# Kernel tuning notes

Hardware: AMD Instinct MI355X
Metric: run time of the kernel (lower is better)

## Reference

```python
import jax, jax.numpy as jnp
import numpy as np

N_NODES = 50000
N_EDGES = 1600000
N_GRAPHS = 1000


def setup_inputs() -> dict:
    key = jax.random.key(0)
    ks = jax.random.split(key, 16)
    s = 0.1
    return {
        "x": jax.random.normal(ks[0], (N_NODES, 7), jnp.float32),
        "edge_attr": jax.random.normal(ks[1], (N_EDGES, 4), jnp.float32),
        "edge_index": jax.random.randint(ks[2], (2, N_EDGES), 0, N_NODES),
        "batch": jnp.sort(jax.random.randint(ks[3], (N_NODES,), 0, N_GRAPHS)),
        "We1": jax.random.normal(ks[4], (4, 7), jnp.float32) * s,
        "be1": jnp.zeros((7,), jnp.float32),
        "W1a": jax.random.normal(ks[5], (7, 64), jnp.float32) * s,
        "b1a": jnp.zeros((64,), jnp.float32),
        "W1b": jax.random.normal(ks[6], (64, 64), jnp.float32) * s,
        "b1b": jnp.zeros((64,), jnp.float32),
        "We2": jax.random.normal(ks[7], (4, 64), jnp.float32) * s,
        "be2": jnp.zeros((64,), jnp.float32),
        "W2a": jax.random.normal(ks[8], (64, 64), jnp.float32) * s,
        "b2a": jnp.zeros((64,), jnp.float32),
        "W2b": jax.random.normal(ks[9], (64, 64), jnp.float32) * s,
        "b2b": jnp.zeros((64,), jnp.float32),
        "Wfc": jax.random.normal(ks[10], (64, 12), jnp.float32) * s,
        "bfc": jnp.zeros((12,), jnp.float32),
    }


def _gine_conv(h, edge_attr, src, dst, We, be, Wa, ba, Wb, bb, n_nodes):
    # GINEConv (eps=0): out = nn(h + sum_j relu(h[src] + lin(edge_attr)))
    e = edge_attr @ We + be                      # [E, d]
    msg = jax.nn.relu(h[src] + e)                # [E, d] gather + add + relu
    aggr = jax.ops.segment_sum(msg, dst, num_segments=n_nodes)  # scatter-sum
    z = h + aggr
    return jax.nn.relu(z @ Wa + ba) @ Wb + bb


def reference(x, edge_attr, edge_index, batch,
              We1, be1, W1a, b1a, W1b, b1b,
              We2, be2, W2a, b2a, W2b, b2b,
              Wfc, bfc):
    src, dst = edge_index[0], edge_index[1]
    n = x.shape[0]
    h = jax.nn.relu(_gine_conv(x, edge_attr, src, dst, We1, be1, W1a, b1a, W1b, b1b, n))
    h = jax.nn.relu(_gine_conv(h, edge_attr, src, dst, We2, be2, W2a, b2a, W2b, b2b, n))
    # global mean pool over batch index
    sums = jax.ops.segment_sum(h, batch, num_segments=N_GRAPHS)          # [G, 64]
    cnt = jax.ops.segment_sum(jnp.ones((n,), h.dtype), batch, num_segments=N_GRAPHS)
    pooled = sums / jnp.maximum(cnt, 1.0)[:, None]
    return pooled @ Wfc + bfc                                            # [G, 12]
```

## Files before the change

kernel.cpp:

```cpp
#include <hip/hip_runtime.h>

typedef unsigned char uchar;
typedef unsigned short ushort;
typedef unsigned int uint;

constexpr int NN = 50000;
constexpr int NE = 1600000;
constexpr int NG = 1000;
constexpr int NB2 = 196;
constexpr int TILE = 4096;
constexpr int NTILE = (NE + TILE - 1) / TILE;
constexpr int SPAN_CAP = 9216;
constexpr int MSTRIDE = 72;
constexpr int NPB = 16;
constexpr int NBLK2 = NN / NPB;

constexpr int OFF_BCNT  = 0;
constexpr int OFF_SUMS  = 256;
constexpr int OFF_CNT   = 64256;
constexpr int ZERO_UNITS= 65280;
constexpr int OFF_BBASE = 65280;
constexpr int OFF_BCUR  = 65536;
constexpr int OFF_OFFS  = 65792;
constexpr int OFF_P0    = 116224;
constexpr int OFF_P1    = 1716224;
constexpr int OFF_P2    = 3316224;
constexpr int OFF_Z1    = 4916224;
constexpr int OFF_H1    = 5316224;
constexpr int OFF_Z     = 6916224;

typedef __attribute__((ext_vector_type(8))) short short8;
typedef __attribute__((ext_vector_type(4))) float float4v;
typedef __attribute__((ext_vector_type(2))) float float2v;

__device__ __forceinline__ uint f2bf(float f) {
    uint u = __float_as_uint(f);
    return (u + 0x7fffu + ((u >> 16) & 1u)) >> 16;
}
__device__ __forceinline__ float bf2f_lo(uint p) { return __uint_as_float(p << 16); }
__device__ __forceinline__ float bf2f_hi(uint p) { return __uint_as_float(p & 0xffff0000u); }

__global__ __launch_bounds__(256) void bhist_kernel(const int* __restrict__ eidx,
                                                    int* __restrict__ bcnt) {
    __shared__ int lh[NB2];
    for (int i = threadIdx.x; i < NB2; i += 256) lh[i] = 0;
    __syncthreads();
    int tid = blockIdx.x * 256 + threadIdx.x;
    int stride = gridDim.x * 256;
    for (int e = tid; e < NE; e += stride) atomicAdd(&lh[eidx[NE + e] >> 8], 1);
    __syncthreads();
    for (int i = threadIdx.x; i < NB2; i += 256) if (lh[i]) atomicAdd(&bcnt[i], lh[i]);
}

__global__ __launch_bounds__(256) void bscan_kernel(const int* __restrict__ bcnt,
                                                    int* __restrict__ bbase,
                                                    int* __restrict__ bcur) {
    __shared__ int s[256];
    int t = threadIdx.x;
    int v = (t < NB2) ? bcnt[t] : 0;
    s[t] = v; __syncthreads();
    for (int o = 1; o < 256; o <<= 1) {
        int u = (t >= o) ? s[t - o] : 0;
        __syncthreads();
        s[t] += u;
        __syncthreads();
    }
    bbase[t] = s[t] - v;
    bcur[t] = s[t] - v;
}

__global__ __launch_bounds__(256) void bin_kernel(const int* __restrict__ eidx,
                                                  const float4* __restrict__ ea,
                                                  int* __restrict__ bcur,
                                                  uint* __restrict__ p0,
                                                  uint* __restrict__ p1,
                                                  uint* __restrict__ p2) {
    __shared__ uint s0[TILE], s1[TILE], s2[TILE];
    __shared__ int hcnt[NB2], hoff[NB2 + 1], hcur[NB2], gbase[NB2];
    const int t = threadIdx.x;
    const int e0 = blockIdx.x * TILE;
    const int cnt = (NE - e0 < TILE) ? (NE - e0) : TILE;
    for (int i = t; i < NB2; i += 256) hcnt[i] = 0;
    __syncthreads();
    int dsts[16];
    #pragma unroll
    for (int k = 0; k < 16; ++k) {
        int i = t + k * 256;
        int d = (i < cnt) ? eidx[NE + e0 + i] : -1;
        dsts[k] = d;
        if (d >= 0) atomicAdd(&hcnt[d >> 8], 1);
    }
    __syncthreads();
    if (t == 0) {
        int a = 0;
        for (int b = 0; b < NB2; ++b) { hoff[b] = a; a += hcnt[b]; }
        hoff[NB2] = a;
    }
    __syncthreads();
    if (t < NB2) { hcur[t] = hoff[t]; gbase[t] = atomicAdd(&bcur[t], hcnt[t]); }
    __syncthreads();
    #pragma unroll
    for (int k = 0; k < 16; ++k) {
        int d = dsts[k];
        if (d < 0) continue;
        int i = t + k * 256;
        int e = e0 + i;
        int src = eidx[e];
        float4 a = ea[e];
        int bkt = d >> 8;
        int lp = atomicAdd(&hcur[bkt], 1);
        s0[lp] = (uint)src | ((uint)(d & 255) << 16) | ((uint)bkt << 24);
        s1[lp] = f2bf(a.x) | (f2bf(a.y) << 16);
        s2[lp] = f2bf(a.z) | (f2bf(a.w) << 16);
    }
    __syncthreads();
    for (int i = t; i < cnt; i += 256) {
        uint r0 = s0[i];
        int bkt = (int)(r0 >> 24);
        int gp = gbase[bkt] + (i - hoff[bkt]);
        p0[gp] = r0; p1[gp] = s1[i]; p2[gp] = s2[i];
    }
}

__global__ __launch_bounds__(256) void build_kernel(const int* __restrict__ bbase,
                                                    const int* __restrict__ bcnt,
                                                    int* __restrict__ offs,
                                                    uint* __restrict__ p0,
                                                    uint* __restrict__ p1,
                                                    uint* __restrict__ p2) {
    __shared__ uint s0[SPAN_CAP], s1[SPAN_CAP], s2[SPAN_CAP];
    __shared__ int ldeg[256], lcur[256], sscan[256];
    const int t = threadIdx.x;
    const int b = blockIdx.x;
    const int nlo = b << 8;
    const int base = bbase[b];
    int span = bcnt[b];
    if (span > SPAN_CAP) span = SPAN_CAP;
    ldeg[t] = 0;
    __syncthreads();
    for (int i = t; i < span; i += 256)
        atomicAdd(&ldeg[(p0[base + i] >> 16) & 0xFFu], 1);
    __syncthreads();
    int v = ldeg[t];
    sscan[t] = v; __syncthreads();
    for (int o = 1; o < 256; o <<= 1) {
        int u = (t >= o) ? sscan[t - o] : 0;
        __syncthreads();
        sscan[t] += u;
        __syncthreads();
    }
    int exc = sscan[t] - v;
    lcur[t] = exc;
    int gi = nlo + t;
    if (gi < NN) offs[gi] = base + exc;
    else if (gi < 50176) offs[gi] = NE;
    __syncthreads();
    for (int i = t; i < span; i += 256) {
        uint r0 = p0[base + i], r1 = p1[base + i], r2 = p2[base + i];
        int pos = atomicAdd(&lcur[(r0 >> 16) & 0xFFu], 1);
        s0[pos] = r0; s1[pos] = r1; s2[pos] = r2;
    }
    __syncthreads();
    for (int i = t; i < span; i += 256) {
        p0[base + i] = s0[i]; p1[base + i] = s1[i]; p2[base + i] = s2[i];
    }
}

__global__ __launch_bounds__(256) void xpack_kernel(const float* __restrict__ x,
                                                    float* __restrict__ xp) {
    int i = blockIdx.x * 256 + threadIdx.x;
    if (i < NN * 8) {
        int n = i >> 3, c = i & 7;
        xp[i] = (c < 7) ? x[n * 7 + c] : 0.f;
    }
}

__global__ __launch_bounds__(256) void aggr1_kernel(
    const float* __restrict__ xp,
    const uint* __restrict__ p0, const uint* __restrict__ p1, const uint* __restrict__ p2,
    const int* __restrict__ offs,
    const float* __restrict__ We1, const float* __restrict__ be1,
    float* __restrict__ z1)
{
    const int tid = threadIdx.x;
    const int lane = tid & 63;
    const int wv = tid >> 6;
    const int grp = lane >> 2;
    const int cl = lane & 3;
    const int n = blockIdx.x * 64 + wv * 16 + grp;

    float2v wE[4], bE;
    const bool c1ok = (2 * cl + 1 < 7);
    #pragma unroll
    for (int k = 0; k < 4; ++k) {
        wE[k][0] = We1[k * 7 + 2 * cl];
        wE[k][1] = c1ok ? We1[k * 7 + 2 * cl + 1] : 0.f;
    }
    bE[0] = be1[2 * cl];
    bE[1] = c1ok ? be1[2 * cl + 1] : 0.f;

    const int off = offs[n];
    const int deg = offs[n + 1] - off;
    const int degm1 = (deg > 0) ? deg - 1 : 0;
    const int offC = (deg > 0) ? off : 0;
    int dmax = deg;
    dmax = max(dmax, __shfl_xor(dmax, 4));
    dmax = max(dmax, __shfl_xor(dmax, 8));
    dmax = max(dmax, __shfl_xor(dmax, 16));
    dmax = max(dmax, __shfl_xor(dmax, 32));

    float2v acc = {0.f, 0.f};
    const float2v zero2 = {0.f, 0.f};
    int j = 0;
    for (; j + 2 <= dmax; j += 2) {
        const bool q0 = (j < deg), q1 = (j + 1 < deg);
        const int e0 = offC + (q0 ? j : degm1);
        const int e1 = offC + (q1 ? j + 1 : degm1);
        const uint r00 = p0[e0], ry0 = p1[e0], rz0 = p2[e0];
        const uint r01 = p0[e1], ry1 = p1[e1], rz1 = p2[e1];
        const float2v xg0 = *(const float2v*)&xp[((size_t)(r00 & 0xFFFFu) << 3) + 2 * cl];
        const float2v xg1 = *(const float2v*)&xp[((size_t)(r01 & 0xFFFFu) << 3) + 2 * cl];
        {
            float2v ev = bE + bf2f_lo(ry0) * wE[0] + bf2f_hi(ry0) * wE[1]
                       + bf2f_lo(rz0) * wE[2] + bf2f_hi(rz0) * wE[3];
            float2v tv = xg0 + ev;
            tv[0] = fmaxf(tv[0], 0.f);
            tv[1] = fmaxf(tv[1], 0.f);
            acc += q0 ? tv : zero2;
        }
        {
            float2v ev = bE + bf2f_lo(ry1) * wE[0] + bf2f_hi(ry1) * wE[1]
                       + bf2f_lo(rz1) * wE[2] + bf2f_hi(rz1) * wE[3];
            float2v tv = xg1 + ev;
            tv[0] = fmaxf(tv[0], 0.f);
            tv[1] = fmaxf(tv[1], 0.f);
            acc += q1 ? tv : zero2;
        }
    }
    if (j < dmax) {
        const bool q0 = (j < deg);
        const int e0 = offC + (q0 ? j : degm1);
        const uint r00 = p0[e0], ry0 = p1[e0], rz0 = p2[e0];
        const float2v xg0 = *(const float2v*)&xp[((size_t)(r00 & 0xFFFFu) << 3) + 2 * cl];
        float2v ev = bE + bf2f_lo(ry0) * wE[0] + bf2f_hi(ry0) * wE[1]
                   + bf2f_lo(rz0) * wE[2] + bf2f_hi(rz0) * wE[3];
        float2v tv = xg0 + ev;
        tv[0] = fmaxf(tv[0], 0.f);
        tv[1] = fmaxf(tv[1], 0.f);
        acc += q0 ? tv : zero2;
    }

    if (n < NN) {
        const float2v xn = *(const float2v*)&xp[(size_t)n * 8 + 2 * cl];
        float2v zv = xn + acc;
        *(float2v*)&z1[(size_t)n * 8 + 2 * cl] = zv;
    }
}

__global__ __launch_bounds__(256) void node1_kernel(
    const float* __restrict__ z1,
    const float* __restrict__ W1a, const float* __restrict__ b1a,
    const float* __restrict__ W1b, const float* __restrict__ b1b,
    uint* __restrict__ h1u)
{
    __shared__ __align__(16) ushort sT[64 * MSTRIDE];
    __shared__ __align__(16) ushort sO[64 * 64];
    const int t = threadIdx.x;
    const int w = t >> 6, lane = t & 63;
    const int qm = lane & 15, quad = lane >> 4;
    const int n0 = blockIdx.x * 64;
    const int node = n0 + w * 16 + qm;

    short8 wa1n[4];
    #pragma unroll
    for (int nt = 0; nt < 4; ++nt) {
        short8 v = (short8)0;
        if (quad == 0) {
            #pragma unroll
            for (int j = 0; j < 7; ++j)
                v[j] = (short)f2bf(W1a[j * 64 + nt * 16 + qm]);
        }
        wa1n[nt] = v;
    }
    short8 wb1[2][4];
    #pragma unroll
    for (int s = 0; s < 2; ++s)
        #pragma unroll
        for (int nt = 0; nt < 4; ++nt) {
            short8 v;
            #pragma unroll
            for (int j = 0; j < 8; ++j)
                v[j] = (short)f2bf(W1b[(s * 32 + quad * 8 + j) * 64 + nt * 16 + qm]);
            wb1[s][nt] = v;
        }
    float ba[4], bb[4];
    #pragma unroll
    for (int nt = 0; nt < 4; ++nt) { ba[nt] = b1a[nt * 16 + qm]; bb[nt] = b1b[nt * 16 + qm]; }

    short8 af1 = (short8)0;
    if (quad == 0 && node < NN) {
        const float4 za = *(const float4*)(z1 + (size_t)node * 8);
        const float4 zbv = *(const float4*)(z1 + (size_t)node * 8 + 4);
        af1[0] = (short)f2bf(za.x); af1[1] = (short)f2bf(za.y);
        af1[2] = (short)f2bf(za.z); af1[3] = (short)f2bf(za.w);
        af1[4] = (short)f2bf(zbv.x); af1[5] = (short)f2bf(zbv.y);
        af1[6] = (short)f2bf(zbv.z); af1[7] = (short)f2bf(zbv.w);
    }
    float4v acc[4];
    #pragma unroll
    for (int nt = 0; nt < 4; ++nt) {
        acc[nt] = (float4v){0.f, 0.f, 0.f, 0.f};
        acc[nt] = __builtin_amdgcn_mfma_f32_16x16x32_bf16(af1, wa1n[nt], acc[nt], 0, 0, 0);
    }
    #pragma unroll
    for (int nt = 0; nt < 4; ++nt)
        #pragma unroll
        for (int r = 0; r < 4; ++r)
            sT[(w * 16 + quad * 4 + r) * MSTRIDE + nt * 16 + qm] =
                (ushort)f2bf(fmaxf(acc[nt][r] + ba[nt], 0.f));
    __syncthreads();

    #pragma unroll
    for (int nt = 0; nt < 4; ++nt) acc[nt] = (float4v){0.f, 0.f, 0.f, 0.f};
    #pragma unroll
    for (int s = 0; s < 2; ++s) {
        short8 af = *(const short8*)&sT[(w * 16 + qm) * MSTRIDE + s * 32 + quad * 8];
        #pragma unroll
        for (int nt = 0; nt < 4; ++nt)
            acc[nt] = __builtin_amdgcn_mfma_f32_16x16x32_bf16(af, wb1[s][nt], acc[nt], 0, 0, 0);
    }
    #pragma unroll
    for (int nt = 0; nt < 4; ++nt)
        #pragma unroll
        for (int r = 0; r < 4; ++r)
            sO[(w * 16 + quad * 4 + r) * 64 + nt * 16 + qm] =
                (ushort)f2bf(fmaxf(acc[nt][r] + bb[nt], 0.f));
    __syncthreads();
    for (int i = t; i < 64 * 32; i += 256) {
        int nd = i >> 5;
        if (n0 + nd < NN) h1u[(size_t)(n0 + nd) * 32 + (i & 31)] = ((const uint*)sO)[i];
    }
}

__global__ __launch_bounds__(256) void aggr2_kernel(
    const uint* __restrict__ h1u,
    const uint* __restrict__ p0, const uint* __restrict__ p1, const uint* __restrict__ p2,
    const int* __restrict__ offs,
    const float* __restrict__ We2, const float* __restrict__ be2,
    uint* __restrict__ zb)
{
    const int tid = threadIdx.x;
    const int lane = tid & 63;
    const int wv = tid >> 6;
    const int grp = lane >> 4;
    const int cl = lane & 15;
    const int n = blockIdx.x * NPB + wv * 4 + grp;

    float2v wA[4], wB[4], bA, bB;
    #pragma unroll
    for (int k = 0; k < 4; ++k) {
        const float4 w4 = *(const float4*)&We2[k * 64 + 4 * cl];
        wA[k][0] = w4.x; wA[k][1] = w4.y;
        wB[k][0] = w4.z; wB[k][1] = w4.w;
    }
    {
        const float4 b4 = *(const float4*)&be2[4 * cl];
        bA[0] = b4.x; bA[1] = b4.y;
        bB[0] = b4.z; bB[1] = b4.w;
    }

    const int off = offs[n];
    const int deg = offs[n + 1] - off;
    const int degm1 = (deg > 0) ? deg - 1 : 0;
    const int offC = (deg > 0) ? off : 0;
    int dmax = deg;
    dmax = max(dmax, __shfl_xor(dmax, 16));
    dmax = max(dmax, __shfl_xor(dmax, 32));

    float2v accA = {0.f, 0.f}, accB = {0.f, 0.f};
    const float2v zero2 = {0.f, 0.f};
    int j = 0;
    for (; j + 2 <= dmax; j += 2) {
        const bool q0 = (j < deg), q1 = (j + 1 < deg);
        const int e0 = offC + (q0 ? j : degm1);
        const int e1 = offC + (q1 ? j + 1 : degm1);
        const uint r00 = p0[e0], ry0 = p1[e0], rz0 = p2[e0];
        const uint r01 = p0[e1], ry1 = p1[e1], rz1 = p2[e1];
        const uint2 g0 = *(const uint2*)&h1u[((size_t)(r00 & 0xFFFFu) << 5) + 2 * cl];
        const uint2 g1 = *(const uint2*)&h1u[((size_t)(r01 & 0xFFFFu) << 5) + 2 * cl];
        {
            float2v bvA = bA + bf2f_lo(ry0) * wA[0] + bf2f_hi(ry0) * wA[1]
                        + bf2f_lo(rz0) * wA[2] + bf2f_hi(rz0) * wA[3];
            float2v bvB = bB + bf2f_lo(ry0) * wB[0] + bf2f_hi(ry0) * wB[1]
                        + bf2f_lo(rz0) * wB[2] + bf2f_hi(rz0) * wB[3];
            float2v tA, tB;
            tA[0] = fmaxf(bf2f_lo(g0.x) + bvA[0], 0.f);
            tA[1] = fmaxf(bf2f_hi(g0.x) + bvA[1], 0.f);
            tB[0] = fmaxf(bf2f_lo(g0.y) + bvB[0], 0.f);
            tB[1] = fmaxf(bf2f_hi(g0.y) + bvB[1], 0.f);
            accA += q0 ? tA : zero2;
            accB += q0 ? tB : zero2;
        }
        {
            float2v bvA = bA + bf2f_lo(ry1) * wA[0] + bf2f_hi(ry1) * wA[1]
                        + bf2f_lo(rz1) * wA[2] + bf2f_hi(rz1) * wA[3];
            float2v bvB = bB + bf2f_lo(ry1) * wB[0] + bf2f_hi(ry1) * wB[1]
                        + bf2f_lo(rz1) * wB[2] + bf2f_hi(rz1) * wB[3];
            float2v tA, tB;
            tA[0] = fmaxf(bf2f_lo(g1.x) + bvA[0], 0.f);
            tA[1] = fmaxf(bf2f_hi(g1.x) + bvA[1], 0.f);
            tB[0] = fmaxf(bf2f_lo(g1.y) + bvB[0], 0.f);
            tB[1] = fmaxf(bf2f_hi(g1.y) + bvB[1], 0.f);
            accA += q1 ? tA : zero2;
            accB += q1 ? tB : zero2;
        }
    }
    if (j < dmax) {
        const bool q0 = (j < deg);
        const int e0 = offC + (q0 ? j : degm1);
        const uint r00 = p0[e0], ry0 = p1[e0], rz0 = p2[e0];
        const uint2 g0 = *(const uint2*)&h1u[((size_t)(r00 & 0xFFFFu) << 5) + 2 * cl];
        float2v bvA = bA + bf2f_lo(ry0) * wA[0] + bf2f_hi(ry0) * wA[1]
                    + bf2f_lo(rz0) * wA[2] + bf2f_hi(rz0) * wA[3];
        float2v bvB = bB + bf2f_lo(ry0) * wB[0] + bf2f_hi(ry0) * wB[1]
                    + bf2f_lo(rz0) * wB[2] + bf2f_hi(rz0) * wB[3];
        float2v tA, tB;
        tA[0] = fmaxf(bf2f_lo(g0.x) + bvA[0], 0.f);
        tA[1] = fmaxf(bf2f_hi(g0.x) + bvA[1], 0.f);
        tB[0] = fmaxf(bf2f_lo(g0.y) + bvB[0], 0.f);
        tB[1] = fmaxf(bf2f_hi(g0.y) + bvB[1], 0.f);
        accA += q0 ? tA : zero2;
        accB += q0 ? tB : zero2;
    }

    const uint2 hw = *(const uint2*)&h1u[(size_t)n * 32 + 2 * cl];
    uint o0 = f2bf(bf2f_lo(hw.x) + accA[0]) | (f2bf(bf2f_hi(hw.x) + accA[1]) << 16);
    uint o1 = f2bf(bf2f_lo(hw.y) + accB[0]) | (f2bf(bf2f_hi(hw.y) + accB[1]) << 16);
    uint2 ov; ov.x = o0; ov.y = o1;
    *(uint2*)&zb[(size_t)n * 32 + 2 * cl] = ov;
}

__global__ __launch_bounds__(256) void mlp2_kernel(
    const uint* __restrict__ zb,
    const float* __restrict__ W2a, const float* __restrict__ b2a,
    const float* __restrict__ W2b, const float* __restrict__ b2b,
    const int* __restrict__ batch,
    float* __restrict__ sums, float* __restrict__ cnt)
{
    __shared__ __align__(16) ushort sT[64 * MSTRIDE];
    __shared__ float sH[64 * 64];
    __shared__ int sB[64];
    __shared__ float pbuf[4][64];
    __shared__ int pcnt[4];
    const int t = threadIdx.x;
    const int w = t >> 6, lane = t & 63;
    const int qm = lane & 15, quad = lane >> 4;
    const int n0 = blockIdx.x * 64;
    const int node = n0 + w * 16 + qm;
    const int nv = (NN - n0 < 64) ? (NN - n0) : 64;

    if (t < 64) sB[t] = (n0 + t < NN) ? batch[n0 + t] : -2;

    short8 wa[2][4], wb[2][4];
    #pragma unroll
    for (int s = 0; s < 2; ++s)
        #pragma unroll
        for (int nt = 0; nt < 4; ++nt) {
            short8 va, vb;
            #pragma unroll
            for (int j = 0; j < 8; ++j) {
                int k = s * 32 + quad * 8 + j, n = nt * 16 + qm;
                va[j] = (short)f2bf(W2a[k * 64 + n]);
                vb[j] = (short)f2bf(W2b[k * 64 + n]);
            }
            wa[s][nt] = va; wb[s][nt] = vb;
        }
    float ba[4], bb[4];
    #pragma unroll
    for (int nt = 0; nt < 4; ++nt) { ba[nt] = b2a[nt * 16 + qm]; bb[nt] = b2b[nt * 16 + qm]; }

    float4v acc[4];
    #pragma unroll
    for (int nt = 0; nt < 4; ++nt) acc[nt] = (float4v){0.f, 0.f, 0.f, 0.f};
    #pragma unroll
    for (int s = 0; s < 2; ++s) {
        uint4 zw = (node < NN) ? *(const uint4*)&zb[(size_t)node * 32 + s * 16 + quad * 4]
                               : make_uint4(0, 0, 0, 0);
        short8 af;
        *(uint4*)&af = zw;
        #pragma unroll
        for (int nt = 0; nt < 4; ++nt)
            acc[nt] = __builtin_amdgcn_mfma_f32_16x16x32_bf16(af, wa[s][nt], acc[nt], 0, 0, 0);
    }
    #pragma unroll
    for (int nt = 0; nt < 4; ++nt)
        #pragma unroll
        for (int r = 0; r < 4; ++r)
            sT[(w * 16 + quad * 4 + r) * MSTRIDE + nt * 16 + qm] =
                (ushort)f2bf(fmaxf(acc[nt][r] + ba[nt], 0.f));
    __syncthreads();

    #pragma unroll
    for (int nt = 0; nt < 4; ++nt) acc[nt] = (float4v){0.f, 0.f, 0.f, 0.f};
    #pragma unroll
    for (int s = 0; s < 2; ++s) {
        short8 af = *(const short8*)&sT[(w * 16 + qm) * MSTRIDE + s * 32 + quad * 8];
        #pragma unroll
        for (int nt = 0; nt < 4; ++nt)
            acc[nt] = __builtin_amdgcn_mfma_f32_16x16x32_bf16(af, wb[s][nt], acc[nt], 0, 0, 0);
    }
    #pragma unroll
    for (int nt = 0; nt < 4; ++nt)
        #pragma unroll
        for (int r = 0; r < 4; ++r)
            sH[(w * 16 + quad * 4 + r) * 64 + nt * 16 + qm] = fmaxf(acc[nt][r] + bb[nt], 0.f);
    __syncthreads();

    const int glo = sB[0];
    const int ghi = sB[nv - 1];
    const int c = t >> 6, d = t & 63;
    for (int g = glo; g <= ghi; ++g) {
        float p = 0.f;
        int lc = 0;
        #pragma unroll 4
        for (int i = 0; i < 16; ++i) {
            int nd = c * 16 + i;
            if (sB[nd] == g) { p += sH[nd * 64 + d]; ++lc; }
        }
        pbuf[c][d] = p;
        if (d == 0) pcnt[c] = lc;
        __syncthreads();
        int tc = pcnt[0] + pcnt[1] + pcnt[2] + pcnt[3];
        if (tc > 0) {
            if (c == 0) {
                float tot = pbuf[0][d] + pbuf[1][d] + pbuf[2][d] + pbuf[3][d];
                atomicAdd(&sums[(size_t)g * 64 + d], tot);
            }
            if (t == 0) atomicAdd(&cnt[g], (float)tc);
        }
        __syncthreads();
    }
}

__global__ __launch_bounds__(256) void fc_kernel(
    const float* __restrict__ sums, const float* __restrict__ cnt,
    const float* __restrict__ Wfc, const float* __restrict__ bfc,
    float* __restrict__ out)
{
    int gid = blockIdx.x * blockDim.x + threadIdx.x;
    if (gid >= NG * 12) return;
    int g = gid / 12, jj = gid - g * 12;
    float inv = 1.f / fmaxf(cnt[g], 1.f);
    float acc = bfc[jj];
    #pragma unroll 8
    for (int k = 0; k < 64; ++k) acc += sums[(size_t)g * 64 + k] * inv * Wfc[k * 12 + jj];
    out[gid] = acc;
}

extern "C" void kernel_launch(void* const* d_in, const int* in_sizes, int n_in,
                              void* d_out, int out_size, void* d_ws, size_t ws_size,
                              hipStream_t stream)
{
    (void)in_sizes; (void)n_in; (void)out_size; (void)ws_size;
    const float*  x    = (const float*)d_in[0];
    const float4* ea   = (const float4*)d_in[1];
    const int*    eidx = (const int*)d_in[2];
    const int*    batch= (const int*)d_in[3];
    const float*  We1  = (const float*)d_in[4];
    const float*  be1  = (const float*)d_in[5];
    const float*  W1a  = (const float*)d_in[6];
    const float*  b1a  = (const float*)d_in[7];
    const float*  W1b  = (const float*)d_in[8];
    const float*  b1b  = (const float*)d_in[9];
    const float*  We2  = (const float*)d_in[10];
    const float*  be2  = (const float*)d_in[11];
    const float*  W2a  = (const float*)d_in[12];
    const float*  b2a  = (const float*)d_in[13];
    const float*  W2b  = (const float*)d_in[14];
    const float*  b2b  = (const float*)d_in[15];
    const float*  Wfc  = (const float*)d_in[16];
    const float*  bfc  = (const float*)d_in[17];
    float* out = (float*)d_out;
    float* ws  = (float*)d_ws;

    int*   bcnt  = (int*)(ws + OFF_BCNT);
    float* sums  = ws + OFF_SUMS;
    float* cnt   = ws + OFF_CNT;
    int*   bbase = (int*)(ws + OFF_BBASE);
    int*   bcur  = (int*)(ws + OFF_BCUR);
    int*   offs  = (int*)(ws + OFF_OFFS);
    uint*  p0    = (uint*)(ws + OFF_P0);
    uint*  p1    = (uint*)(ws + OFF_P1);
    uint*  p2    = (uint*)(ws + OFF_P2);
    float* z1    = ws + OFF_Z1;
    uint*  h1u   = (uint*)(ws + OFF_H1);
    uint*  zb    = (uint*)(ws + OFF_Z);
    float* xp    = ws + OFF_Z;

    hipMemsetAsync(d_ws, 0, (size_t)ZERO_UNITS * 4, stream);

    bhist_kernel<<<256, 256, 0, stream>>>(eidx, bcnt);
    bscan_kernel<<<1, 256, 0, stream>>>(bcnt, bbase, bcur);
    bin_kernel  <<<NTILE, 256, 0, stream>>>(eidx, ea, bcur, p0, p1, p2);
    build_kernel<<<NB2, 256, 0, stream>>>(bbase, bcnt, offs, p0, p1, p2);
    xpack_kernel<<<(NN * 8 + 255) / 256, 256, 0, stream>>>(x, xp);
    aggr1_kernel<<<(NN + 63) / 64, 256, 0, stream>>>(xp, p0, p1, p2, offs, We1, be1, z1);
    node1_kernel<<<(NN + 63) / 64, 256, 0, stream>>>(z1, W1a, b1a, W1b, b1b, h1u);
    aggr2_kernel<<<NBLK2, 256, 0, stream>>>(h1u, p0, p1, p2, offs, We2, be2, zb);
    mlp2_kernel <<<(NN + 63) / 64, 256, 0, stream>>>(zb, W2a, b2a, W2b, b2b, batch, sums, cnt);
    fc_kernel   <<<(NG * 12 + 255) / 256, 256, 0, stream>>>(sums, cnt, Wfc, bfc, out);
}
```

Measured before the change: 294.0 us.

## Sort nodes by degree to balance edge aggregation across wavefront lanes

Adds a degree histogram, scan and scatter that produce a degree-sorted node permutation. Both aggregation kernels then look up their node through this permutation, so the nodes sharing a wavefront have similar edge counts and lanes idle less in the max-degree loop. The degree-sort scratch reuses the pooled-sums region, so that region is re-zeroed before the pooling kernel. The cost is three extra small launches plus a memset, and the aggregation kernels lose locality in their node reads and writes.

```diff
diff --git a/kernel.cpp b/kernel.cpp
--- a/kernel.cpp
+++ b/kernel.cpp
@@ -166,6 +166,49 @@
     }
 }
 
+__global__ __launch_bounds__(256) void dhist_kernel(const int* __restrict__ offs,
+                                                    int* __restrict__ dhist) {
+    __shared__ int lh[256];
+    lh[threadIdx.x] = 0;
+    __syncthreads();
+    int i = blockIdx.x * 256 + threadIdx.x;
+    int stride = gridDim.x * 256;
+    for (int n = i; n < NN; n += stride) {
+        int d = offs[n + 1] - offs[n];
+        d = (d < 255) ? d : 255;
+        atomicAdd(&lh[d], 1);
+    }
+    __syncthreads();
+    if (lh[threadIdx.x]) atomicAdd(&dhist[threadIdx.x], lh[threadIdx.x]);
+}
+
+__global__ __launch_bounds__(256) void dscan_kernel(const int* __restrict__ dhist,
+                                                    int* __restrict__ dcur) {
+    __shared__ int s[256];
+    int t = threadIdx.x;
+    int v = dhist[t];
+    s[t] = v; __syncthreads();
+    for (int o = 1; o < 256; o <<= 1) {
+        int u = (t >= o) ? s[t - o] : 0;
+        __syncthreads();
+        s[t] += u;
+        __syncthreads();
+    }
+    dcur[t] = s[t] - v;
+}
+
+__global__ __launch_bounds__(256) void dscat_kernel(const int* __restrict__ offs,
+                                                    int* __restrict__ dcur,
+                                                    int* __restrict__ nsorted) {
+    int n = blockIdx.x * 256 + threadIdx.x;
+    if (n < NN) {
+        int d = offs[n + 1] - offs[n];
+        d = (d < 255) ? d : 255;
+        int pos = atomicAdd(&dcur[d], 1);
+        nsorted[pos] = n;
+    }
+}
+
 __global__ __launch_bounds__(256) void xpack_kernel(const float* __restrict__ x,
                                                     float* __restrict__ xp) {
     int i = blockIdx.x * 256 + threadIdx.x;
@@ -178,7 +221,7 @@
 __global__ __launch_bounds__(256) void aggr1_kernel(
     const float* __restrict__ xp,
     const uint* __restrict__ p0, const uint* __restrict__ p1, const uint* __restrict__ p2,
-    const int* __restrict__ offs,
+    const int* __restrict__ offs, const int* __restrict__ nsorted,
     const float* __restrict__ We1, const float* __restrict__ be1,
     float* __restrict__ z1)
 {
@@ -187,7 +230,8 @@
     const int wv = tid >> 6;
     const int grp = lane >> 2;
     const int cl = lane & 3;
-    const int n = blockIdx.x * 64 + wv * 16 + grp;
+    const int idx = blockIdx.x * 64 + wv * 16 + grp;
+    const int n = (idx < NN) ? nsorted[idx] : NN;
 
     float2v wE[4], bE;
     const bool c1ok = (2 * cl + 1 < 7);
@@ -345,7 +389,7 @@
 __global__ __launch_bounds__(256) void aggr2_kernel(
     const uint* __restrict__ h1u,
     const uint* __restrict__ p0, const uint* __restrict__ p1, const uint* __restrict__ p2,
-    const int* __restrict__ offs,
+    const int* __restrict__ offs, const int* __restrict__ nsorted,
     const float* __restrict__ We2, const float* __restrict__ be2,
     uint* __restrict__ zb)
 {
@@ -354,7 +398,7 @@
     const int wv = tid >> 6;
     const int grp = lane >> 4;
     const int cl = lane & 15;
-    const int n = blockIdx.x * NPB + wv * 4 + grp;
+    const int n = nsorted[blockIdx.x * NPB + wv * 4 + grp];
 
     float2v wA[4], wB[4], bA, bB;
     #pragma unroll
@@ -596,6 +640,9 @@
     uint*  h1u   = (uint*)(ws + OFF_H1);
     uint*  zb    = (uint*)(ws + OFF_Z);
     float* xp    = ws + OFF_Z;
+    int*   dhist = (int*)(ws + OFF_SUMS);
+    int*   dcur  = (int*)(ws + OFF_SUMS + 256);
+    int*   nsorted = (int*)(ws + OFF_SUMS + 1024);
 
     hipMemsetAsync(d_ws, 0, (size_t)ZERO_UNITS * 4, stream);
 
@@ -603,10 +650,14 @@
     bscan_kernel<<<1, 256, 0, stream>>>(bcnt, bbase, bcur);
     bin_kernel  <<<NTILE, 256, 0, stream>>>(eidx, ea, bcur, p0, p1, p2);
     build_kernel<<<NB2, 256, 0, stream>>>(bbase, bcnt, offs, p0, p1, p2);
+    dhist_kernel<<<64, 256, 0, stream>>>(offs, dhist);
+    dscan_kernel<<<1, 256, 0, stream>>>(dhist, dcur);
+    dscat_kernel<<<(NN + 255) / 256, 256, 0, stream>>>(offs, dcur, nsorted);
     xpack_kernel<<<(NN * 8 + 255) / 256, 256, 0, stream>>>(x, xp);
-    aggr1_kernel<<<(NN + 63) / 64, 256, 0, stream>>>(xp, p0, p1, p2, offs, We1, be1, z1);
+    aggr1_kernel<<<(NN + 63) / 64, 256, 0, stream>>>(xp, p0, p1, p2, offs, nsorted, We1, be1, z1);
     node1_kernel<<<(NN + 63) / 64, 256, 0, stream>>>(z1, W1a, b1a, W1b, b1b, h1u);
-    aggr2_kernel<<<NBLK2, 256, 0, stream>>>(h1u, p0, p1, p2, offs, We2, be2, zb);
+    aggr2_kernel<<<NBLK2, 256, 0, stream>>>(h1u, p0, p1, p2, offs, nsorted, We2, be2, zb);
+    hipMemsetAsync(ws + OFF_SUMS, 0, (size_t)64000 * 4, stream);
     mlp2_kernel <<<(NN + 63) / 64, 256, 0, stream>>>(zb, W2a, b2a, W2b, b2b, batch, sums, cnt);
     fc_kernel   <<<(NG * 12 + 255) / 256, 256, 0, stream>>>(sums, cnt, Wfc, bfc, out);
 }
```

Result: slower. 389.4 us (+32.5%).

## Sort nodes by degree within buckets to balance aggregation warps

Applied to the files above, without the earlier changes.

The build kernel now computes a per-256-node counting sort by in-degree and writes a node permutation (nsorted). Both aggregation kernels read nodes through this permutation, so the lanes of one wavefront handle nodes of similar degree and the max-degree loop wastes fewer iterations. The permutation buffer reuses the sums area of the workspace, so an extra memset re-zeroes sums before mlp2. This adds a scan in build_kernel, an indirect node lookup, and scattered writes to z1 and zb.

```diff
diff --git a/kernel.cpp b/kernel.cpp
--- a/kernel.cpp
+++ b/kernel.cpp
@@ -125,6 +125,7 @@
 __global__ __launch_bounds__(256) void build_kernel(const int* __restrict__ bbase,
                                                     const int* __restrict__ bcnt,
                                                     int* __restrict__ offs,
+                                                    int* __restrict__ nsorted,
                                                     uint* __restrict__ p0,
                                                     uint* __restrict__ p1,
                                                     uint* __restrict__ p2) {
@@ -164,6 +165,25 @@
     for (int i = t; i < span; i += 256) {
         p0[base + i] = s0[i]; p1[base + i] = s1[i]; p2[base + i] = s2[i];
     }
+
+    __syncthreads();
+    const int key = (gi < NN) ? ((v < 255) ? v : 254) : 255;
+    ldeg[t] = 0;
+    __syncthreads();
+    atomicAdd(&ldeg[key], 1);
+    __syncthreads();
+    int v2 = ldeg[t];
+    sscan[t] = v2; __syncthreads();
+    for (int o = 1; o < 256; o <<= 1) {
+        int u = (t >= o) ? sscan[t - o] : 0;
+        __syncthreads();
+        sscan[t] += u;
+        __syncthreads();
+    }
+    lcur[t] = sscan[t] - v2;
+    __syncthreads();
+    int r = atomicAdd(&lcur[key], 1);
+    nsorted[nlo + r] = gi;
 }
 
 __global__ __launch_bounds__(256) void xpack_kernel(const float* __restrict__ x,
@@ -178,7 +198,7 @@
 __global__ __launch_bounds__(256) void aggr1_kernel(
     const float* __restrict__ xp,
     const uint* __restrict__ p0, const uint* __restrict__ p1, const uint* __restrict__ p2,
-    const int* __restrict__ offs,
+    const int* __restrict__ offs, const int* __restrict__ nsorted,
     const float* __restrict__ We1, const float* __restrict__ be1,
     float* __restrict__ z1)
 {
@@ -187,7 +207,8 @@
     const int wv = tid >> 6;
     const int grp = lane >> 2;
     const int cl = lane & 3;
-    const int n = blockIdx.x * 64 + wv * 16 + grp;
+    const int idx = blockIdx.x * 64 + wv * 16 + grp;
+    const int n = nsorted[idx];
 
     float2v wE[4], bE;
     const bool c1ok = (2 * cl + 1 < 7);
@@ -200,7 +221,7 @@
     bE[1] = c1ok ? be1[2 * cl + 1] : 0.f;
 
     const int off = offs[n];
-    const int deg = offs[n + 1] - off;
+    const int deg = (n < NN) ? (offs[n + 1] - off) : 0;
     const int degm1 = (deg > 0) ? deg - 1 : 0;
     const int offC = (deg > 0) ? off : 0;
     int dmax = deg;
@@ -345,7 +366,7 @@
 __global__ __launch_bounds__(256) void aggr2_kernel(
     const uint* __restrict__ h1u,
     const uint* __restrict__ p0, const uint* __restrict__ p1, const uint* __restrict__ p2,
-    const int* __restrict__ offs,
+    const int* __restrict__ offs, const int* __restrict__ nsorted,
     const float* __restrict__ We2, const float* __restrict__ be2,
     uint* __restrict__ zb)
 {
@@ -354,7 +375,7 @@
     const int wv = tid >> 6;
     const int grp = lane >> 4;
     const int cl = lane & 15;
-    const int n = blockIdx.x * NPB + wv * 4 + grp;
+    const int n = nsorted[blockIdx.x * NPB + wv * 4 + grp];
 
     float2v wA[4], wB[4], bA, bB;
     #pragma unroll
@@ -596,17 +617,19 @@
     uint*  h1u   = (uint*)(ws + OFF_H1);
     uint*  zb    = (uint*)(ws + OFF_Z);
     float* xp    = ws + OFF_Z;
+    int*   nsorted = (int*)(ws + OFF_SUMS + 1024);
 
     hipMemsetAsync(d_ws, 0, (size_t)ZERO_UNITS * 4, stream);
 
     bhist_kernel<<<256, 256, 0, stream>>>(eidx, bcnt);
     bscan_kernel<<<1, 256, 0, stream>>>(bcnt, bbase, bcur);
     bin_kernel  <<<NTILE, 256, 0, stream>>>(eidx, ea, bcur, p0, p1, p2);
-    build_kernel<<<NB2, 256, 0, stream>>>(bbase, bcnt, offs, p0, p1, p2);
+    build_kernel<<<NB2, 256, 0, stream>>>(bbase, bcnt, offs, nsorted, p0, p1, p2);
     xpack_kernel<<<(NN * 8 + 255) / 256, 256, 0, stream>>>(x, xp);
-    aggr1_kernel<<<(NN + 63) / 64, 256, 0, stream>>>(xp, p0, p1, p2, offs, We1, be1, z1);
+    aggr1_kernel<<<(50176) / 64, 256, 0, stream>>>(xp, p0, p1, p2, offs, nsorted, We1, be1, z1);
     node1_kernel<<<(NN + 63) / 64, 256, 0, stream>>>(z1, W1a, b1a, W1b, b1b, h1u);
-    aggr2_kernel<<<NBLK2, 256, 0, stream>>>(h1u, p0, p1, p2, offs, We2, be2, zb);
+    aggr2_kernel<<<NBLK2, 256, 0, stream>>>(h1u, p0, p1, p2, offs, nsorted, We2, be2, zb);
+    hipMemsetAsync(ws + OFF_SUMS, 0, (size_t)64000 * 4, stream);
     mlp2_kernel <<<(NN + 63) / 64, 256, 0, stream>>>(zb, W2a, b2a, W2b, b2b, batch, sums, cnt);
     fc_kernel   <<<(NG * 12 + 255) / 256, 256, 0, stream>>>(sums, cnt, Wfc, bfc, out);
 }
```

New measurement: 310.0 us. +5.5%, slower.
